# Kernel tuning notes

Hardware: AMD Instinct MI355X
Metric: run time of the kernel (lower is better)

## Reference

```python
import jax, jax.numpy as jnp
import numpy as np

B, S, D, H = 16, 1024, 768, 12
HS = D // H  # head size = 64
NEG = -1000000.0  # module uses -1e6, not -inf


def setup_inputs() -> dict:
    key = jax.random.key(0)
    k1, k2, k3 = jax.random.split(key, 3)
    scale = 1.0 / np.sqrt(D)
    return {
        "x": jax.random.normal(k1, (B, S, D), dtype=jnp.float32),
        "W_qkv": jax.random.normal(k2, (D, 3 * D), dtype=jnp.float32) * scale,
        "b_qkv": jnp.zeros((3 * D,), dtype=jnp.float32),
        "W_o": jax.random.normal(k3, (D, D), dtype=jnp.float32) * scale,
        "b_o": jnp.zeros((D,), dtype=jnp.float32),
    }


def reference(x, W_qkv, b_qkv, W_o, b_o):
    qkv = x @ W_qkv + b_qkv                      # [B,S,3D]
    q, k, v = jnp.split(qkv, 3, axis=-1)         # each [B,S,D]
    q = q.reshape(B, S, H, HS)
    k = k.reshape(B, S, H, HS)
    v = v.reshape(B, S, H, HS)
    scores = jnp.einsum('bqhd,bkhd->bhqk', q, k) / np.sqrt(HS).astype(np.float32)
    causal = jnp.tril(jnp.ones((S, S), dtype=bool))
    scores = jnp.where(causal, scores, jnp.float32(NEG))
    probs = jax.nn.softmax(scores, axis=-1)      # dropout is eval-mode identity
    av = jnp.einsum('bhqk,bkhd->bqhd', probs, v).reshape(B, S, D)
    return av @ W_o + b_o
```

## Files before the change

### kernel.cpp

```cpp
#include <hip/hip_runtime.h>
#include <stdint.h>

typedef unsigned short u16;
typedef __attribute__((ext_vector_type(8))) short bf16x8;
typedef __attribute__((ext_vector_type(8))) u16 u16x8;
typedef __attribute__((ext_vector_type(4))) u16 u16x4;
typedef __attribute__((ext_vector_type(4))) float f32x4;
typedef __attribute__((ext_vector_type(16))) float f32x16;

#define B_ 16
#define S_ 1024
#define D_ 768
#define H_ 12

__device__ __forceinline__ float bf2f(u16 u) {
  unsigned int x = ((unsigned int)u) << 16;
  float f;
  __builtin_memcpy(&f, &x, 4);
  return f;
}
__device__ __forceinline__ u16 f2bf(float f) {
  unsigned int x;
  __builtin_memcpy(&x, &f, 4);
  x += 0x7fffu + ((x >> 16) & 1u);
  return (u16)(x >> 16);
}

#define MFMA16(a, b, c) __builtin_amdgcn_mfma_f32_16x16x32_bf16((a), (b), (c), 0, 0, 0)
#define MFMA32(a, b, c) __builtin_amdgcn_mfma_f32_32x32x16_bf16((a), (b), (c), 0, 0, 0)

#define GLD16(g, l)                                              \
  __builtin_amdgcn_global_load_lds(                              \
      (const __attribute__((address_space(1))) void*)(g),        \
      (__attribute__((address_space(3))) void*)(l), 16, 0, 0)

__global__ __launch_bounds__(256) void cvt_bf16(const float* __restrict__ in,
                                                u16* __restrict__ out, int n8) {
  const int i = blockIdx.x * 256 + threadIdx.x;
  if (i >= n8) return;
  const float4 a = *(const float4*)(in + (size_t)i * 8);
  const float4 b = *(const float4*)(in + (size_t)i * 8 + 4);
  u16x8 o;
  o[0] = f2bf(a.x); o[1] = f2bf(a.y); o[2] = f2bf(a.z); o[3] = f2bf(a.w);
  o[4] = f2bf(b.x); o[5] = f2bf(b.y); o[6] = f2bf(b.z); o[7] = f2bf(b.w);
  *(u16x8*)(out + (size_t)i * 8) = o;
}

__global__ __launch_bounds__(256) void transpose_cvt(const float* __restrict__ W,
                                                     u16* __restrict__ Wt, int K, int N) {
  __shared__ u16 t[32][33];
  const int n0 = blockIdx.x * 32, k0 = blockIdx.y * 32;
  const int tx = threadIdx.x & 31, ty = threadIdx.x >> 5;
#pragma unroll
  for (int i = 0; i < 32; i += 8)
    t[ty + i][tx] = f2bf(W[(size_t)(k0 + ty + i) * N + n0 + tx]);
  __syncthreads();
#pragma unroll
  for (int i = 0; i < 32; i += 8) Wt[(size_t)(n0 + ty + i) * K + k0 + tx] = t[tx][ty + i];
}

template <int MODE>
__global__ __launch_bounds__(256) void gemm_bt(const u16* __restrict__ A,
                                               const u16* __restrict__ Bt,
                                               const float* __restrict__ bias,
                                               u16* __restrict__ O0, u16* __restrict__ O1,
                                               u16* __restrict__ O2, float* __restrict__ Of,
                                               int M, int N, int K) {
  __shared__ u16 Al[3 * 128 * 32];
  __shared__ u16 Bl[3 * 128 * 32];
  const int tid = threadIdx.x;
  const int wid = tid >> 6, lane = tid & 63;
  const int lo = lane & 15, hi = lane >> 4;
  const int wr = wid >> 1, wc = wid & 1;
  const int m0 = blockIdx.x * 128, n0 = blockIdx.y * 128;
  const int rA = lane >> 2;
  const int kc = (lane & 3) * 8;
  const int srow = wid * 16 + rA;
  f32x4 acc[4][4] = {};
  const int kiters = K >> 5;

  const u16* agp0 = A + (size_t)(m0 + srow) * K + kc;
  const u16* agp1 = A + (size_t)(m0 + srow + 64) * K + kc;
  const u16* bgp0 = Bt + (size_t)(n0 + srow) * K + kc;
  const u16* bgp1 = Bt + (size_t)(n0 + srow + 64) * K + kc;
  const int wb = wid * 1024;

#define STAGE(kt, buf)                                          \
  do {                                                          \
    const int _k0 = (kt) * 32;                                  \
    const int _nb = (buf) * 8192;    \
    GLD16(agp0 + _k0, (char*)Al + _nb + wb);                    \
    GLD16(agp1 + _k0, (char*)Al + _nb + 4096 + wb);             \
    GLD16(bgp0 + _k0, (char*)Bl + _nb + wb);                    \
    GLD16(bgp1 + _k0, (char*)Bl + _nb + 4096 + wb);             \
  } while (0)

  STAGE(0, 0);
  STAGE(1, 1);
  asm volatile("s_waitcnt vmcnt(4)" ::: "memory");
  __builtin_amdgcn_s_barrier();

  for (int kt = 0; kt < kiters; ++kt) {
    const bool st = (kt + 2 < kiters);
    if (st) STAGE(kt + 2, (kt + 2) % 3);
    const int cb = (kt % 3) * 4096;
    bf16x8 af[4], bfr[4];
#pragma unroll
    for (int i = 0; i < 4; ++i)
      af[i] = *(const bf16x8*)&Al[cb + (wr * 64 + i * 16 + lo) * 32 + hi * 8];
#pragma unroll
    for (int j = 0; j < 4; ++j)
      bfr[j] = *(const bf16x8*)&Bl[cb + (wc * 64 + j * 16 + lo) * 32 + hi * 8];
    __builtin_amdgcn_s_setprio(1);
#pragma unroll
    for (int i = 0; i < 4; ++i)
#pragma unroll
      for (int j = 0; j < 4; ++j) acc[i][j] = MFMA16(af[i], bfr[j], acc[i][j]);
    __builtin_amdgcn_s_setprio(0);
    if (st) {
      asm volatile("s_waitcnt vmcnt(4)" ::: "memory");
    } else if (kt + 1 < kiters) {
      asm volatile("s_waitcnt vmcnt(0)" ::: "memory");
    }
    __builtin_amdgcn_s_barrier();
  }
#undef STAGE
#pragma unroll
  for (int j = 0; j < 4; ++j) {
    const int n = n0 + wc * 64 + j * 16 + lo;
    const float bv = bias[n];
#pragma unroll
    for (int i = 0; i < 4; ++i) {
#pragma unroll
      for (int r = 0; r < 4; ++r) {
        const int m = m0 + wr * 64 + i * 16 + hi * 4 + r;
        const float fv = acc[i][j][r] + bv;
        if (MODE == 0) {
          const u16 o = f2bf(fv);
          if (n0 < D_) {
            O0[(size_t)m * D_ + n] = o;
          } else if (n0 < 2 * D_) {
            O1[(size_t)m * D_ + (n - D_)] = o;
          } else {
            const int np = n - 2 * D_;
            O2[(((size_t)(m >> 10) * H_ + (np >> 6)) * 64 + (np & 63)) * S_ + (m & 1023)] = o;
          }
        } else {
          Of[(size_t)m * N + n] = fv;
        }
      }
    }
  }
}

__global__ __launch_bounds__(256) void attn_fwd2(const u16* __restrict__ Qb,
                                                 const u16* __restrict__ Kb,
                                                 const u16* __restrict__ VTb,
                                                 u16* __restrict__ att) {
  __shared__ u16 Kl[2048];
  __shared__ u16 Vl[2048];
  const int tid = threadIdx.x;
  const int lane = tid & 63, wid = tid >> 6;
  const int l31 = lane & 31, hi1 = lane >> 5;
  const int L = blockIdx.x + 8 * (blockIdx.y + 12 * blockIdx.z);
  const int bx = (L >> 3) & 7;
  const int P = (L & 7) + 8 * (L >> 6);
  const int h = P % 12, b = P / 12;
  const int q0 = bx * 128;
  const int qw0 = q0 + wid * 32;
  const int qg = qw0 + l31;
  const size_t rowbase = (size_t)b * S_;

  bf16x8 qf[4];
  {
    const u16* qp = Qb + (rowbase + qg) * D_ + h * 64 + hi1 * 8;
#pragma unroll
    for (int c = 0; c < 4; ++c) {
      bf16x8 v = *(const bf16x8*)(qp + c * 16);
#pragma unroll
      for (int j = 0; j < 8; ++j) v[j] = (short)f2bf(bf2f((u16)v[j]) * 0.125f);
      qf[c] = v;
    }
  }
  float mrun = -3.0e38f, lrun = 0.0f;
  f32x16 o0 = {}, o1 = {};

  const u16* kgp =
      Kb + (rowbase + (tid & 31)) * D_ + h * 64 + (tid >> 6) * 16 + ((tid >> 5) & 1) * 8;
  const u16* vgp = VTb +
                   (((size_t)b * H_ + h) * 64 + ((tid >> 6) & 1) * 32 + (tid & 31)) * S_ +
                   (tid >> 7) * 16 + ((tid >> 5) & 1) * 8;
  char* kdst = (char*)Kl + wid * 1024;
  char* vdst = (char*)Vl + wid * 1024;
  const char* kbase = (const char*)Kl + lane * 16;
  const char* vbase = (const char*)Vl + lane * 16;

  const int kvend = q0 + 128;
  for (int kv0 = 0; kv0 < kvend; kv0 += 32) {
    __syncthreads();
    GLD16(kgp + (size_t)kv0 * D_, kdst);
    GLD16(vgp + kv0, vdst);
    __syncthreads();
    if (kv0 > qw0 + 31) continue;

    f32x16 s = {};
#pragma unroll
    for (int c = 0; c < 4; ++c) s = MFMA32(*(const bf16x8*)(kbase + c * 1024), qf[c], s);

    if (kv0 + 31 > qw0) {
#pragma unroll
      for (int r = 0; r < 16; ++r) {
        const int kvg = kv0 + (r & 3) + 8 * (r >> 2) + 4 * hi1;
        if (kvg > qg) s[r] = -1.0e30f;
      }
    }
    float rm = s[0];
#pragma unroll
    for (int r = 1; r < 16; ++r) rm = fmaxf(rm, s[r]);
    rm = fmaxf(rm, __shfl_xor(rm, 32));
    const float mn = fmaxf(mrun, rm);
    const float fr = __expf(mrun - mn);
    mrun = mn;
    float p[16];
    float rs = 0.0f;
#pragma unroll
    for (int r = 0; r < 16; ++r) {
      p[r] = __expf(s[r] - mn);
      rs += p[r];
    }
    rs += __shfl_xor(rs, 32);
    lrun = lrun * fr + rs;
#pragma unroll
    for (int r = 0; r < 16; ++r) {
      o0[r] *= fr;
      o1[r] *= fr;
    }
    unsigned int pa[4], pb[4];
#pragma unroll
    for (int g = 0; g < 4; ++g) {
      pa[g] = (unsigned)f2bf(p[4 * g]) | ((unsigned)f2bf(p[4 * g + 1]) << 16);
      pb[g] = (unsigned)f2bf(p[4 * g + 2]) | ((unsigned)f2bf(p[4 * g + 3]) << 16);
    }
    const unsigned sa = __shfl_xor(hi1 ? pa[0] : pa[1], 32);
    const unsigned sb = __shfl_xor(hi1 ? pb[0] : pb[1], 32);
    const unsigned sc = __shfl_xor(hi1 ? pa[2] : pa[3], 32);
    const unsigned sd = __shfl_xor(hi1 ? pb[2] : pb[3], 32);
    const uint4 w0 = hi1 ? make_uint4(sa, sb, pa[1], pb[1]) : make_uint4(pa[0], pb[0], sa, sb);
    const uint4 w1 = hi1 ? make_uint4(sc, sd, pa[3], pb[3]) : make_uint4(pa[2], pb[2], sc, sd);
    bf16x8 pf0, pf1;
    __builtin_memcpy(&pf0, &w0, 16);
    __builtin_memcpy(&pf1, &w1, 16);
    o0 = MFMA32(*(const bf16x8*)(vbase + 0 * 1024), pf0, o0);
    o1 = MFMA32(*(const bf16x8*)(vbase + 1 * 1024), pf0, o1);
    o0 = MFMA32(*(const bf16x8*)(vbase + 2 * 1024), pf1, o0);
    o1 = MFMA32(*(const bf16x8*)(vbase + 3 * 1024), pf1, o1);
  }
  const float inv = 1.0f / lrun;
  u16* op = att + (rowbase + qg) * D_ + h * 64;
#pragma unroll
  for (int g = 0; g < 4; ++g) {
    u16x4 v0, v1;
#pragma unroll
    for (int j = 0; j < 4; ++j) {
      v0[j] = f2bf(o0[4 * g + j] * inv);
      v1[j] = f2bf(o1[4 * g + j] * inv);
    }
    *(u16x4*)(op + 8 * g + 4 * hi1) = v0;
    *(u16x4*)(op + 32 + 8 * g + 4 * hi1) = v1;
  }
}

extern "C" void kernel_launch(void* const* d_in, const int* in_sizes, int n_in, void* d_out,
                              int out_size, void* d_ws, size_t ws_size, hipStream_t stream) {
  const float *x = nullptr, *Wqkv = nullptr, *bqkv = nullptr, *Wo = nullptr, *bo = nullptr;
  for (int i = 0; i < n_in; ++i) {
    switch (in_sizes[i]) {
      case 16384 * 768:  x = (const float*)d_in[i]; break;
      case 768 * 2304:   Wqkv = (const float*)d_in[i]; break;
      case 2304:         bqkv = (const float*)d_in[i]; break;
      case 768 * 768:    Wo = (const float*)d_in[i]; break;
      case 768:          bo = (const float*)d_in[i]; break;
    }
  }
  float* out = (float*)d_out;

  char* ws = (char*)d_ws;
  u16* WqkvT = (u16*)(ws);
  u16* WoT = (u16*)(ws + 3538944);
  u16* Qb = (u16*)(ws + 4718592);
  u16* Kb = (u16*)(ws + 29884416);
  u16* VT = (u16*)(ws + 55050240);
  u16* xb = (u16*)d_out;
  u16* att = Qb;

  cvt_bf16<<<(16384 * 768 / 8 + 255) / 256, 256, 0, stream>>>(x, xb, 16384 * 768 / 8);
  transpose_cvt<<<dim3(2304 / 32, 768 / 32), 256, 0, stream>>>(Wqkv, WqkvT, 768, 2304);
  transpose_cvt<<<dim3(768 / 32, 768 / 32), 256, 0, stream>>>(Wo, WoT, 768, 768);
  gemm_bt<0><<<dim3(16384 / 128, 2304 / 128), 256, 0, stream>>>(
      xb, WqkvT, bqkv, Qb, Kb, VT, nullptr, 16384, 2304, 768);
  attn_fwd2<<<dim3(8, H_, B_), 256, 0, stream>>>(Qb, Kb, VT, att);
  gemm_bt<1><<<dim3(16384 / 128, 768 / 128), 256, 0, stream>>>(
      att, WoT, bo, nullptr, nullptr, nullptr, out, 16384, 768, 768);
}
```

Measured before the change: 254.2 us.

## Enlarge GEMM tile to 256x128 with 512 threads and fuse prep kernels

The GEMM block grows to 256 rows by 128 columns with eight waves, so each B tile in LDS is shared by twice as many rows and fewer global loads are issued per output. Launch bounds are raised to 512 threads. The input conversion and the two weight transposes are merged into one prep kernel to cut launch overhead. The risks are lower occupancy from the larger LDS use and a coarser grid that may balance poorly across CUs.

```diff
diff --git a/kernel.cpp b/kernel.cpp
--- a/kernel.cpp
+++ b/kernel.cpp
@@ -34,80 +34,94 @@
       (const __attribute__((address_space(1))) void*)(g),        \
       (__attribute__((address_space(3))) void*)(l), 16, 0, 0)
 
-__global__ __launch_bounds__(256) void cvt_bf16(const float* __restrict__ in,
-                                                u16* __restrict__ out, int n8) {
-  const int i = blockIdx.x * 256 + threadIdx.x;
-  if (i >= n8) return;
-  const float4 a = *(const float4*)(in + (size_t)i * 8);
-  const float4 b = *(const float4*)(in + (size_t)i * 8 + 4);
-  u16x8 o;
-  o[0] = f2bf(a.x); o[1] = f2bf(a.y); o[2] = f2bf(a.z); o[3] = f2bf(a.w);
-  o[4] = f2bf(b.x); o[5] = f2bf(b.y); o[6] = f2bf(b.z); o[7] = f2bf(b.w);
-  *(u16x8*)(out + (size_t)i * 8) = o;
-}
-
-__global__ __launch_bounds__(256) void transpose_cvt(const float* __restrict__ W,
-                                                     u16* __restrict__ Wt, int K, int N) {
-  __shared__ u16 t[32][33];
-  const int n0 = blockIdx.x * 32, k0 = blockIdx.y * 32;
-  const int tx = threadIdx.x & 31, ty = threadIdx.x >> 5;
-#pragma unroll
-  for (int i = 0; i < 32; i += 8)
-    t[ty + i][tx] = f2bf(W[(size_t)(k0 + ty + i) * N + n0 + tx]);
-  __syncthreads();
-#pragma unroll
-  for (int i = 0; i < 32; i += 8) Wt[(size_t)(n0 + ty + i) * K + k0 + tx] = t[tx][ty + i];
+__global__ __launch_bounds__(256) void prep(const float* __restrict__ x,
+                                            u16* __restrict__ xb,
+                                            const float* __restrict__ Wqkv,
+                                            u16* __restrict__ WqkvT,
+                                            const float* __restrict__ Wo,
+                                            u16* __restrict__ WoT) {
+  __shared__ u16 tt[32][33];
+  const int gx = blockIdx.x;
+  const int tid = threadIdx.x;
+  if (gx < 6144) {
+    const int i = gx * 256 + tid;
+    const float4 a = *(const float4*)(x + (size_t)i * 8);
+    const float4 b = *(const float4*)(x + (size_t)i * 8 + 4);
+    u16x8 o;
+    o[0] = f2bf(a.x); o[1] = f2bf(a.y); o[2] = f2bf(a.z); o[3] = f2bf(a.w);
+    o[4] = f2bf(b.x); o[5] = f2bf(b.y); o[6] = f2bf(b.z); o[7] = f2bf(b.w);
+    *(u16x8*)(xb + (size_t)i * 8) = o;
+  } else if (gx < 6144 + 1728) {
+    const int t = gx - 6144;
+    const int n0 = (t % 72) * 32, k0 = (t / 72) * 32;
+    const int tx = tid & 31, ty = tid >> 5;
+#pragma unroll
+    for (int i = 0; i < 32; i += 8)
+      tt[ty + i][tx] = f2bf(Wqkv[(size_t)(k0 + ty + i) * 2304 + n0 + tx]);
+    __syncthreads();
+#pragma unroll
+    for (int i = 0; i < 32; i += 8)
+      WqkvT[(size_t)(n0 + ty + i) * 768 + k0 + tx] = tt[tx][ty + i];
+  } else {
+    const int t = gx - 7872;
+    const int n0 = (t % 24) * 32, k0 = (t / 24) * 32;
+    const int tx = tid & 31, ty = tid >> 5;
+#pragma unroll
+    for (int i = 0; i < 32; i += 8)
+      tt[ty + i][tx] = f2bf(Wo[(size_t)(k0 + ty + i) * 768 + n0 + tx]);
+    __syncthreads();
+#pragma unroll
+    for (int i = 0; i < 32; i += 8)
+      WoT[(size_t)(n0 + ty + i) * 768 + k0 + tx] = tt[tx][ty + i];
+  }
 }
 
 template <int MODE>
-__global__ __launch_bounds__(256) void gemm_bt(const u16* __restrict__ A,
-                                               const u16* __restrict__ Bt,
-                                               const float* __restrict__ bias,
-                                               u16* __restrict__ O0, u16* __restrict__ O1,
-                                               u16* __restrict__ O2, float* __restrict__ Of,
-                                               int M, int N, int K) {
-  __shared__ u16 Al[3 * 128 * 32];
+__global__ __launch_bounds__(512, 4) void gemm_bt(const u16* __restrict__ A,
+                                                  const u16* __restrict__ Bt,
+                                                  const float* __restrict__ bias,
+                                                  u16* __restrict__ O0, u16* __restrict__ O1,
+                                                  u16* __restrict__ O2, float* __restrict__ Of,
+                                                  int M, int N, int K) {
+  __shared__ u16 Al[3 * 256 * 32];
   __shared__ u16 Bl[3 * 128 * 32];
   const int tid = threadIdx.x;
   const int wid = tid >> 6, lane = tid & 63;
   const int lo = lane & 15, hi = lane >> 4;
   const int wr = wid >> 1, wc = wid & 1;
-  const int m0 = blockIdx.x * 128, n0 = blockIdx.y * 128;
+  const int m0 = blockIdx.x * 256, n0 = blockIdx.y * 128;
   const int rA = lane >> 2;
   const int kc = (lane & 3) * 8;
   const int srow = wid * 16 + rA;
   f32x4 acc[4][4] = {};
-  const int kiters = K >> 5;
+  const int T = K >> 5;
 
   const u16* agp0 = A + (size_t)(m0 + srow) * K + kc;
-  const u16* agp1 = A + (size_t)(m0 + srow + 64) * K + kc;
+  const u16* agp1 = A + (size_t)(m0 + srow + 128) * K + kc;
   const u16* bgp0 = Bt + (size_t)(n0 + srow) * K + kc;
-  const u16* bgp1 = Bt + (size_t)(n0 + srow + 64) * K + kc;
   const int wb = wid * 1024;
 
-#define STAGE(kt, buf)                                          \
-  do {                                                          \
-    const int _k0 = (kt) * 32;                                  \
-    const int _nb = (buf) * 8192;    \
-    GLD16(agp0 + _k0, (char*)Al + _nb + wb);                    \
-    GLD16(agp1 + _k0, (char*)Al + _nb + 4096 + wb);             \
-    GLD16(bgp0 + _k0, (char*)Bl + _nb + wb);                    \
-    GLD16(bgp1 + _k0, (char*)Bl + _nb + 4096 + wb);             \
+#define STAGE(kt, buf)                                            \
+  do {                                                            \
+    const int _k0 = (kt) * 32;                                    \
+    GLD16(agp0 + _k0, (char*)Al + (buf) * 16384 + wb);            \
+    GLD16(agp1 + _k0, (char*)Al + (buf) * 16384 + 8192 + wb);     \
+    GLD16(bgp0 + _k0, (char*)Bl + (buf) * 8192 + wb);             \
   } while (0)
 
   STAGE(0, 0);
   STAGE(1, 1);
-  asm volatile("s_waitcnt vmcnt(4)" ::: "memory");
+  asm volatile("s_waitcnt vmcnt(3)" ::: "memory");
   __builtin_amdgcn_s_barrier();
 
-  for (int kt = 0; kt < kiters; ++kt) {
-    const bool st = (kt + 2 < kiters);
-    if (st) STAGE(kt + 2, (kt + 2) % 3);
-    const int cb = (kt % 3) * 4096;
+  for (int t = 0; t < T; ++t) {
+    if (t + 2 < T) STAGE(t + 2, (t + 2) % 3);
+    const int ca = (t % 3) * 8192;
+    const int cb = (t % 3) * 4096;
     bf16x8 af[4], bfr[4];
 #pragma unroll
     for (int i = 0; i < 4; ++i)
-      af[i] = *(const bf16x8*)&Al[cb + (wr * 64 + i * 16 + lo) * 32 + hi * 8];
+      af[i] = *(const bf16x8*)&Al[ca + (wr * 64 + i * 16 + lo) * 32 + hi * 8];
 #pragma unroll
     for (int j = 0; j < 4; ++j)
       bfr[j] = *(const bf16x8*)&Bl[cb + (wc * 64 + j * 16 + lo) * 32 + hi * 8];
@@ -117,24 +131,24 @@
 #pragma unroll
       for (int j = 0; j < 4; ++j) acc[i][j] = MFMA16(af[i], bfr[j], acc[i][j]);
     __builtin_amdgcn_s_setprio(0);
-    if (st) {
-      asm volatile("s_waitcnt vmcnt(4)" ::: "memory");
-    } else if (kt + 1 < kiters) {
+    if (t + 2 < T) {
+      asm volatile("s_waitcnt vmcnt(3)" ::: "memory");
+    } else if (t + 1 < T) {
       asm volatile("s_waitcnt vmcnt(0)" ::: "memory");
     }
     __builtin_amdgcn_s_barrier();
   }
 #undef STAGE
 #pragma unroll
-  for (int j = 0; j < 4; ++j) {
-    const int n = n0 + wc * 64 + j * 16 + lo;
+  for (int g = 0; g < 4; ++g) {
+    const int n = n0 + wc * 64 + g * 16 + lo;
     const float bv = bias[n];
 #pragma unroll
-    for (int i = 0; i < 4; ++i) {
+    for (int f = 0; f < 4; ++f) {
 #pragma unroll
       for (int r = 0; r < 4; ++r) {
-        const int m = m0 + wr * 64 + i * 16 + hi * 4 + r;
-        const float fv = acc[i][j][r] + bv;
+        const int m = m0 + wr * 64 + f * 16 + hi * 4 + r;
+        const float fv = acc[f][g][r] + bv;
         if (MODE == 0) {
           const u16 o = f2bf(fv);
           if (n0 < D_) {
@@ -293,12 +307,10 @@
   u16* xb = (u16*)d_out;
   u16* att = Qb;
 
-  cvt_bf16<<<(16384 * 768 / 8 + 255) / 256, 256, 0, stream>>>(x, xb, 16384 * 768 / 8);
-  transpose_cvt<<<dim3(2304 / 32, 768 / 32), 256, 0, stream>>>(Wqkv, WqkvT, 768, 2304);
-  transpose_cvt<<<dim3(768 / 32, 768 / 32), 256, 0, stream>>>(Wo, WoT, 768, 768);
-  gemm_bt<0><<<dim3(16384 / 128, 2304 / 128), 256, 0, stream>>>(
-      xb, WqkvT, bqkv, Qb, Kb, VT, nullptr, 16384, 2304, 768);
+  prep<<<8448, 256, 0, stream>>>(x, xb, Wqkv, WqkvT, Wo, WoT);
+  gemm_bt<0><<<dim3(64, 18), 512, 0, stream>>>(xb, WqkvT, bqkv, Qb, Kb, VT, nullptr,
+                                               16384, 2304, 768);
   attn_fwd2<<<dim3(8, H_, B_), 256, 0, stream>>>(Qb, Kb, VT, att);
-  gemm_bt<1><<<dim3(16384 / 128, 768 / 128), 256, 0, stream>>>(
-      att, WoT, bo, nullptr, nullptr, nullptr, out, 16384, 768, 768);
-}
+  gemm_bt<1><<<dim3(64, 6), 512, 0, stream>>>(att, WoT, bo, nullptr, nullptr, nullptr, out,
+                                              16384, 768, 768);
+}
```

Result: slower. 261.3 us (+2.8%).
